# Kernel tuning notes

Hardware: AMD Instinct MI355X
Metric: run time of the kernel (lower is better)

## Reference

```python
import jax, jax.numpy as jnp
import numpy as np

N_SAMPLES = 128
AGENTS = 64
D = 128          # latent_size
EDIM = 2         # edge attr dim
N = N_SAMPLES * AGENTS
EPS = 1e-5


def _build_edges():
    a = np.arange(AGENTS)
    rows = np.repeat(a, AGENTS)
    cols = np.tile(a, AGENTS)
    mask = rows != cols  # fully connected, no self loops
    rows, cols = rows[mask], cols[mask]
    offsets = (np.arange(N_SAMPLES) * AGENTS)[:, None]
    src = (rows[None, :] + offsets).ravel().astype(np.int32)  # edge_index[0]
    dst = (cols[None, :] + offsets).ravel().astype(np.int32)  # edge_index[1]
    return src, dst


def setup_inputs() -> dict:
    key = jax.random.key(0)
    ks = jax.random.split(key, 16)
    src, dst = _build_edges()
    zin = 2 * D + EDIM  # CGConv concat [x_i, x_j, e]
    inp = {
        "gnn_in": jax.random.normal(ks[0], (N, D), jnp.float32),
        "centers": jax.random.normal(ks[1], (N, EDIM), jnp.float32),
        "edge_src": jnp.asarray(src),
        "edge_dst": jnp.asarray(dst),
    }
    for li, base in ((1, 2), (2, 8)):
        inp[f"Wf{li}"] = jax.random.normal(ks[base + 0], (zin, D), jnp.float32) / np.sqrt(zin)
        inp[f"bf{li}"] = jnp.zeros((D,), jnp.float32)
        inp[f"Ws{li}"] = jax.random.normal(ks[base + 1], (zin, D), jnp.float32) / np.sqrt(zin)
        inp[f"bs{li}"] = jnp.zeros((D,), jnp.float32)
        inp[f"gamma{li}"] = jnp.ones((D,), jnp.float32)
        inp[f"beta{li}"] = jnp.zeros((D,), jnp.float32)
    return inp


def _cgconv(x, e, src, dst, Wf, bf, Ws, bs, gamma, beta):
    # message: z = [x_i(target), x_j(source), e]; sigmoid(Wf z) * softplus(Ws z)
    z = jnp.concatenate([x[dst], x[src], e], axis=-1)  # [E, 2D+2]
    m = jax.nn.sigmoid(z @ Wf + bf) * jax.nn.softplus(z @ Ws + bs)
    agg = jax.ops.segment_sum(m, dst, num_segments=N)  # scatter-add at targets
    # batch norm (training-mode batch stats) then residual, as in PyG CGConv
    mu = agg.mean(axis=0)
    var = agg.var(axis=0)
    agg = (agg - mu) * jax.lax.rsqrt(var + EPS) * gamma + beta
    return agg + x


def reference(gnn_in, centers, edge_src, edge_dst,
              Wf1, bf1, Ws1, bs1, gamma1, beta1,
              Wf2, bf2, Ws2, bs2, gamma2, beta2):
    # edge_attr = centers[col] - centers[row]
    e = centers[edge_dst] - centers[edge_src]  # [E, 2]
    x = jax.nn.relu(_cgconv(gnn_in, e, edge_src, edge_dst, Wf1, bf1, Ws1, bs1, gamma1, beta1))
    x = jax.nn.relu(_cgconv(x, e, edge_src, edge_dst, Wf2, bf2, Ws2, bs2, gamma2, beta2))
    return x
```

## Files before the change

### kernel.cpp

```cpp
#include <hip/hip_runtime.h>
#include <hip/hip_bf16.h>

#define NSAMP 128
#define AGENTS 64
#define D 128
#define NN (NSAMP * AGENTS)
#define LOG2E 1.44269504088896340736f
#define LN2   0.69314718055994530942f
#define EPSF  1e-5f

typedef __attribute__((ext_vector_type(8))) short short8;
typedef __attribute__((ext_vector_type(4))) float floatx4;

__device__ __forceinline__ float u2f(unsigned v) {
    float f; __builtin_memcpy(&f, &v, 4); return f;
}
__device__ __forceinline__ unsigned f2u(float f) {
    unsigned v; __builtin_memcpy(&v, &f, 4); return v;
}
__device__ __forceinline__ unsigned short f2bf(float f) {
    unsigned x; __builtin_memcpy(&x, &f, 4);
    return (unsigned short)((x + 0x7FFFu + ((x >> 16) & 1u)) >> 16);
}

__global__ __launch_bounds__(256) void cvt_kernel(
    const float* __restrict__ Wf1, const float* __restrict__ Ws1,
    const float* __restrict__ Wf2, const float* __restrict__ Ws2,
    unsigned short* __restrict__ WT, float* __restrict__ sacc)
{
    int b = blockIdx.x;
    if (b < 64) {
        int rr = b * 16 + (threadIdx.x >> 4);
        int kk = (threadIdx.x & 15) * 8;
        int layer = rr >> 9, rem = rr & 511, arr = rem >> 7, c = rem & 127;
        const float* M = (arr < 2) ? (layer ? Wf2 : Wf1) : (layer ? Ws2 : Ws1);
        int side = arr & 1;
        short8 s;
        #pragma unroll
        for (int j = 0; j < 8; ++j)
            s[j] = (short)f2bf(M[(size_t)(side * 128 + kk + j) * D + c]);
        *(short8*)&WT[(size_t)(layer * 4 + arr) * 16384 + c * 128 + kk] = s;
    } else {
        sacc[threadIdx.x]       = 0.f;
        sacc[256 + threadIdx.x] = 0.f;
    }
}

__device__ __forceinline__ void stats_tree(
    unsigned int (*EApk)[17], unsigned int (*EBpk)[17],
    int cl, int slot, int c, float s1, float s2, float* __restrict__ sc)
{
    __syncthreads();
    EApk[slot][cl] = f2u(s1);
    EBpk[slot][cl] = f2u(s2);
    __syncthreads();
    #pragma unroll
    for (int off = 8; off >= 1; off >>= 1) {
        if (slot < off) {
            EApk[slot][cl] = f2u(u2f(EApk[slot][cl]) + u2f(EApk[slot + off][cl]));
            EBpk[slot][cl] = f2u(u2f(EBpk[slot][cl]) + u2f(EBpk[slot + off][cl]));
        }
        __syncthreads();
    }
    if (slot == 0) {
        atomicAdd(&sc[c],       u2f(EApk[0][cl]));
        atomicAdd(&sc[128 + c], u2f(EBpk[0][cl]));
    }
}

template<int LAYER>
__global__ __launch_bounds__(256, 4) void prep_half(
    const float* __restrict__ xin,
    const float* __restrict__ agg_in,
    const unsigned short* __restrict__ WT,
    const float* __restrict__ centers,
    const float* __restrict__ Wf, const float* __restrict__ bf_,
    const float* __restrict__ Ws, const float* __restrict__ bs_,
    const float* __restrict__ gm_prev, const float* __restrict__ bt_prev,
    const float* __restrict__ sacc_prev,
    float* __restrict__ agg_out, float* __restrict__ sacc_out)
{
    const int bid = blockIdx.x;
    const int xcd = bid & 7;
    const int tmp = bid >> 3;
    const int inner = tmp & 15;
    const int s = ((tmp >> 4) << 3) + xcd;
    const int q = inner >> 1, h = inner & 1;

    const int nbase = s * AGENTS;
    const int tid = threadIdx.x, w = tid >> 6, lane = tid & 63;
    const int quad = lane >> 4, l16 = lane & 15;
    const int col = q * 16 + l16;

    __shared__ unsigned int EApk[32][17];
    __shared__ unsigned int EBpk[64][17];
    __shared__ float bnA[128], bnB[128];

    if (LAYER == 2) {
        if (tid < 128) {
            const float inv = 1.f / NN;
            float mu = sacc_prev[tid] * inv;
            float var = sacc_prev[128 + tid] * inv - mu * mu;
            float rs = rsqrtf(var + EPSF);
            float A = rs * gm_prev[tid];
            bnA[tid] = A;
            bnB[tid] = fmaf(-mu, A, bt_prev[tid]);
        }
        __syncthreads();
    }

    short8 a[4];
    if (LAYER == 1) {
        const float* xr = xin + (size_t)(nbase + w * 16 + l16) * D + quad * 8;
        #pragma unroll
        for (int kc = 0; kc < 4; ++kc) {
            float4 v0 = *(const float4*)(xr + kc * 32);
            float4 v1 = *(const float4*)(xr + kc * 32 + 4);
            short8 t;
            t[0] = (short)f2bf(v0.x); t[1] = (short)f2bf(v0.y);
            t[2] = (short)f2bf(v0.z); t[3] = (short)f2bf(v0.w);
            t[4] = (short)f2bf(v1.x); t[5] = (short)f2bf(v1.y);
            t[6] = (short)f2bf(v1.z); t[7] = (short)f2bf(v1.w);
            a[kc] = t;
        }
    } else {
        const size_t ro = (size_t)(nbase + w * 16 + l16) * D + quad * 8;
        #pragma unroll
        for (int kc = 0; kc < 4; ++kc) {
            int cc = quad * 8 + kc * 32;
            float4 g0 = *(const float4*)&agg_in[ro + kc * 32];
            float4 g1 = *(const float4*)&agg_in[ro + kc * 32 + 4];
            float4 x0v = *(const float4*)(xin + ro + kc * 32);
            float4 x1v = *(const float4*)(xin + ro + kc * 32 + 4);
            float4 A0 = *(const float4*)&bnA[cc], A1 = *(const float4*)&bnA[cc + 4];
            float4 B0 = *(const float4*)&bnB[cc], B1 = *(const float4*)&bnB[cc + 4];
            short8 t;
            t[0] = (short)f2bf(fmaxf(0.f, fmaf(g0.x, A0.x, B0.x) + x0v.x));
            t[1] = (short)f2bf(fmaxf(0.f, fmaf(g0.y, A0.y, B0.y) + x0v.y));
            t[2] = (short)f2bf(fmaxf(0.f, fmaf(g0.z, A0.z, B0.z) + x0v.z));
            t[3] = (short)f2bf(fmaxf(0.f, fmaf(g0.w, A0.w, B0.w) + x0v.w));
            t[4] = (short)f2bf(fmaxf(0.f, fmaf(g1.x, A1.x, B1.x) + x1v.x));
            t[5] = (short)f2bf(fmaxf(0.f, fmaf(g1.y, A1.y, B1.y) + x1v.y));
            t[6] = (short)f2bf(fmaxf(0.f, fmaf(g1.z, A1.z, B1.z) + x1v.z));
            t[7] = (short)f2bf(fmaxf(0.f, fmaf(g1.w, A1.w, B1.w) + x1v.w));
            a[kc] = t;
        }
    }

    const int doEA = ((w >> 1) == h);
    floatx4 accB[2];
    #pragma unroll
    for (int a2 = 0; a2 < 2; ++a2) {
        const int arr = 1 + 2 * a2;
        const unsigned short* wp = WT + ((size_t)arr * 128 + col) * 128 + quad * 8;
        floatx4 ac = {0.f, 0.f, 0.f, 0.f};
        #pragma unroll
        for (int kc = 0; kc < 4; ++kc)
            ac = __builtin_amdgcn_mfma_f32_16x16x32_bf16(
                a[kc], *(const short8*)(wp + kc * 32), ac, 0, 0, 0);
        accB[a2] = ac;
    }
    floatx4 accA[2] = {{0,0,0,0},{0,0,0,0}};
    if (doEA) {
        #pragma unroll
        for (int a2 = 0; a2 < 2; ++a2) {
            const int arr = 2 * a2;
            const unsigned short* wp = WT + ((size_t)arr * 128 + col) * 128 + quad * 8;
            floatx4 ac = {0.f, 0.f, 0.f, 0.f};
            #pragma unroll
            for (int kc = 0; kc < 4; ++kc)
                ac = __builtin_amdgcn_mfma_f32_16x16x32_bf16(
                    a[kc], *(const short8*)(wp + kc * 32), ac, 0, 0, 0);
            accA[a2] = ac;
        }
    }
    const float cwf0 = Wf[256 * D + col], cwf1 = Wf[257 * D + col];
    const float cws0 = Ws[256 * D + col], cws1 = Ws[257 * D + col];
    const float bfv = bf_[col], bsv = bs_[col];
    #pragma unroll
    for (int r = 0; r < 4; ++r) {
        int row = w * 16 + quad * 4 + r;
        int n = nbase + row;
        float ce0 = centers[2 * n], ce1 = centers[2 * n + 1];
        float ctf = fmaf(ce0, cwf0, ce1 * cwf1);
        float cts = fmaf(ce0, cws0, ce1 * cws1);
        unsigned ebf = (unsigned)f2bf(__builtin_amdgcn_exp2f(-LOG2E * (accB[0][r] - ctf)));
        unsigned ebs = (unsigned)f2bf(__builtin_amdgcn_exp2f( LOG2E * (accB[1][r] - cts)));
        EBpk[row][l16] = ebf | (ebs << 16);
        if (doEA) {
            unsigned eaf = (unsigned)f2bf(__builtin_amdgcn_exp2f(-LOG2E * (accA[0][r] + ctf + bfv)));
            unsigned eas = (unsigned)f2bf(__builtin_amdgcn_exp2f( LOG2E * (accA[1][r] + cts + bsv)));
            EApk[(w & 1) * 16 + quad * 4 + r][l16] = eaf | (eas << 16);
        }
    }
    __syncthreads();

    const int cl = tid & 15, slot = tid >> 4;
    const int c = q * 16 + cl;
    float eaf[2], eas[2], ac2[2];
    #pragma unroll
    for (int i = 0; i < 2; ++i) {
        unsigned pk = EApk[slot * 2 + i][cl];
        eaf[i] = u2f(pk << 16);
        eas[i] = u2f(pk & 0xFFFF0000u);
        ac2[i] = 0.f;
    }
    #pragma unroll
    for (int jb = 0; jb < 64; jb += 8) {
        float ebf[8], ebs[8];
        #pragma unroll
        for (int u = 0; u < 8; ++u) {
            unsigned pk = EBpk[jb + u][cl];
            ebf[u] = u2f(pk << 16);
            ebs[u] = u2f(pk & 0xFFFF0000u);
        }
        float sg[16], lg[16];
        #pragma unroll
        for (int u = 0; u < 8; ++u) {
            sg[u * 2 + 0] = __builtin_amdgcn_rcpf(fmaf(eaf[0], ebf[u], 1.f));
            sg[u * 2 + 1] = __builtin_amdgcn_rcpf(fmaf(eaf[1], ebf[u], 1.f));
            lg[u * 2 + 0] = __builtin_amdgcn_logf(fmaf(eas[0], ebs[u], 1.f));
            lg[u * 2 + 1] = __builtin_amdgcn_logf(fmaf(eas[1], ebs[u], 1.f));
        }
        #pragma unroll
        for (int u = 0; u < 8; ++u) {
            ac2[0] = fmaf(sg[u * 2 + 0], lg[u * 2 + 0], ac2[0]);
            ac2[1] = fmaf(sg[u * 2 + 1], lg[u * 2 + 1], ac2[1]);
        }
    }
    float s1 = 0.f, s2 = 0.f;
    #pragma unroll
    for (int i = 0; i < 2; ++i) {
        int d = h * 32 + slot * 2 + i;
        unsigned pk = EBpk[d][cl];
        float ebf = u2f(pk << 16);
        float ebs = u2f(pk & 0xFFFF0000u);
        float sg = __builtin_amdgcn_rcpf(fmaf(eaf[i], ebf, 1.f));
        float lg = __builtin_amdgcn_logf(fmaf(eas[i], ebs, 1.f));
        float v = (ac2[i] - sg * lg) * LN2;
        agg_out[(size_t)(nbase + d) * D + c] = v;
        s1 += v; s2 += v * v;
    }
    stats_tree(EApk, EBpk, cl, slot, c, s1, s2, sacc_out);
}

__global__ __launch_bounds__(256) void final_bn(
    const float* __restrict__ x0, const float* __restrict__ agg1,
    const float* __restrict__ agg2, const float* __restrict__ sacc,
    const float* __restrict__ gm1, const float* __restrict__ bt1,
    const float* __restrict__ gm2, const float* __restrict__ bt2,
    float* __restrict__ outp)
{
    const int tid = threadIdx.x;
    __shared__ float bnA[128], bnB[128], bn2A[128], bn2B[128];
    if (tid < 128) {
        const float inv = 1.f / NN;
        float mu = sacc[tid] * inv;
        float var = sacc[128 + tid] * inv - mu * mu;
        float rs = rsqrtf(var + EPSF);
        float A = rs * gm1[tid];
        bnA[tid] = A;
        bnB[tid] = fmaf(-mu, A, bt1[tid]);
        float mu2 = sacc[256 + tid] * inv;
        float var2 = sacc[384 + tid] * inv - mu2 * mu2;
        float rs2 = rsqrtf(var2 + EPSF);
        float A2 = rs2 * gm2[tid];
        bn2A[tid] = A2;
        bn2B[tid] = fmaf(-mu2, A2, bt2[tid]);
    }
    __syncthreads();
    const int bid = blockIdx.x;
    const int s = ((bid >> 5) << 3) + (bid & 7);
    const int inner = (bid >> 3) & 3;
    const int t = (s * 4 + inner) * 256 + tid;
    const int n = t >> 4, c8 = (t & 15) * 8;
    size_t off = (size_t)n * D + c8;
    float o[8];
    #pragma unroll
    for (int hh = 0; hh < 2; ++hh) {
        float4 g2 = *(const float4*)&agg2[off + hh * 4];
        float4 g1 = *(const float4*)&agg1[off + hh * 4];
        float4 xv = *(const float4*)&x0[off + hh * 4];
        int cc = c8 + hh * 4;
        o[hh*4+0] = fmaxf(0.f, fmaf(g2.x, bn2A[cc+0], bn2B[cc+0]) +
                    fmaxf(0.f, fmaf(g1.x, bnA[cc+0], bnB[cc+0]) + xv.x));
        o[hh*4+1] = fmaxf(0.f, fmaf(g2.y, bn2A[cc+1], bn2B[cc+1]) +
                    fmaxf(0.f, fmaf(g1.y, bnA[cc+1], bnB[cc+1]) + xv.y));
        o[hh*4+2] = fmaxf(0.f, fmaf(g2.z, bn2A[cc+2], bn2B[cc+2]) +
                    fmaxf(0.f, fmaf(g1.z, bnA[cc+2], bnB[cc+2]) + xv.z));
        o[hh*4+3] = fmaxf(0.f, fmaf(g2.w, bn2A[cc+3], bn2B[cc+3]) +
                    fmaxf(0.f, fmaf(g1.w, bnA[cc+3], bnB[cc+3]) + xv.w));
    }
    *(float4*)&outp[off]     = *(float4*)&o[0];
    *(float4*)&outp[off + 4] = *(float4*)&o[4];
}

extern "C" void kernel_launch(void* const* d_in, const int* in_sizes, int n_in,
                              void* d_out, int out_size, void* d_ws, size_t ws_size,
                              hipStream_t stream) {
    const float* x0      = (const float*)d_in[0];
    const float* centers = (const float*)d_in[1];
    const float* Wf1 = (const float*)d_in[4];
    const float* bf1 = (const float*)d_in[5];
    const float* Ws1 = (const float*)d_in[6];
    const float* bs1 = (const float*)d_in[7];
    const float* gm1 = (const float*)d_in[8];
    const float* bt1 = (const float*)d_in[9];
    const float* Wf2 = (const float*)d_in[10];
    const float* bf2 = (const float*)d_in[11];
    const float* Ws2 = (const float*)d_in[12];
    const float* bs2 = (const float*)d_in[13];
    const float* gm2 = (const float*)d_in[14];
    const float* bt2 = (const float*)d_in[15];

    const size_t ND = (size_t)NN * D;
    unsigned short* WT = (unsigned short*)d_ws;
    float* fbase = (float*)(WT + 2 * 65536);
    float* agg1  = fbase;
    float* agg2  = fbase + ND;
    float* sacc  = fbase + 2 * ND;
    float* outp  = (float*)d_out;

    cvt_kernel<<<dim3(65), dim3(256), 0, stream>>>(
        Wf1, Ws1, Wf2, Ws2, WT, sacc);

    prep_half<1><<<dim3(2048), dim3(256), 0, stream>>>(
        x0, agg1 , WT, centers, Wf1, bf1, Ws1, bs1,
        gm1 , bt1 , sacc , agg1, sacc);

    prep_half<2><<<dim3(2048), dim3(256), 0, stream>>>(
        x0, agg1, WT + 65536, centers, Wf2, bf2, Ws2, bs2,
        gm1, bt1, sacc, agg2, sacc + 256);

    final_bn<<<dim3(512), dim3(256), 0, stream>>>(
        x0, agg1, agg2, sacc, gm1, bt1, gm2, bt2, outp);
}
```

Baseline: 162.6 us.

## Fuse weight bf16 conversion into conv kernels via LDS staging, drop cvt kernel

Removes the separate weight-transpose/convert kernel. Each prep_half block now loads its 16-column fp32 weight slice, converts it to bf16 and stages it in shared memory, and the MFMA B operands read from LDS instead of a global bf16 buffer. The stats accumulator is zeroed with hipMemsetAsync instead of inside that kernel. The sigmoid/softplus inner loop is restructured to precompute its arguments, with rcp/log issued through inline asm. The trade is one fewer launch in exchange for redundant strided fp32 weight loads in each of the 2048 blocks per layer, plus extra LDS use and a barrier.

New measurement: 150.5 us. -7.4%, faster.

```diff
diff --git a/kernel.cpp b/kernel.cpp
--- a/kernel.cpp
+++ b/kernel.cpp
@@ -23,29 +23,6 @@
     return (unsigned short)((x + 0x7FFFu + ((x >> 16) & 1u)) >> 16);
 }
 
-__global__ __launch_bounds__(256) void cvt_kernel(
-    const float* __restrict__ Wf1, const float* __restrict__ Ws1,
-    const float* __restrict__ Wf2, const float* __restrict__ Ws2,
-    unsigned short* __restrict__ WT, float* __restrict__ sacc)
-{
-    int b = blockIdx.x;
-    if (b < 64) {
-        int rr = b * 16 + (threadIdx.x >> 4);
-        int kk = (threadIdx.x & 15) * 8;
-        int layer = rr >> 9, rem = rr & 511, arr = rem >> 7, c = rem & 127;
-        const float* M = (arr < 2) ? (layer ? Wf2 : Wf1) : (layer ? Ws2 : Ws1);
-        int side = arr & 1;
-        short8 s;
-        #pragma unroll
-        for (int j = 0; j < 8; ++j)
-            s[j] = (short)f2bf(M[(size_t)(side * 128 + kk + j) * D + c]);
-        *(short8*)&WT[(size_t)(layer * 4 + arr) * 16384 + c * 128 + kk] = s;
-    } else {
-        sacc[threadIdx.x]       = 0.f;
-        sacc[256 + threadIdx.x] = 0.f;
-    }
-}
-
 __device__ __forceinline__ void stats_tree(
     unsigned int (*EApk)[17], unsigned int (*EBpk)[17],
     int cl, int slot, int c, float s1, float s2, float* __restrict__ sc)
@@ -72,7 +49,6 @@
 __global__ __launch_bounds__(256, 4) void prep_half(
     const float* __restrict__ xin,
     const float* __restrict__ agg_in,
-    const unsigned short* __restrict__ WT,
     const float* __restrict__ centers,
     const float* __restrict__ Wf, const float* __restrict__ bf_,
     const float* __restrict__ Ws, const float* __restrict__ bs_,
@@ -92,10 +68,25 @@
     const int quad = lane >> 4, l16 = lane & 15;
     const int col = q * 16 + l16;
 
+    __shared__ __align__(16) unsigned short WL[4][16][136];
     __shared__ unsigned int EApk[32][17];
     __shared__ unsigned int EBpk[64][17];
     __shared__ float bnA[128], bnB[128];
 
+    {
+        const int arr = tid >> 6, klane = tid & 63;
+        const int wcol = klane & 15, kg = klane >> 4;
+        const float* M = (arr < 2) ? Wf : Ws;
+        const int side = arr & 1;
+        const float* src = M + (size_t)(side * 128 + kg * 32) * D + q * 16 + wcol;
+        #pragma unroll
+        for (int u = 0; u < 16; ++u) {
+            float f0 = src[(size_t)(2 * u) * D];
+            float f1 = src[(size_t)(2 * u + 1) * D];
+            unsigned pk = (unsigned)f2bf(f0) | ((unsigned)f2bf(f1) << 16);
+            *(unsigned*)&WL[arr][wcol][kg * 32 + 2 * u] = pk;
+        }
+    }
     if (LAYER == 2) {
         if (tid < 128) {
             const float inv = 1.f / NN;
@@ -106,8 +97,8 @@
             bnA[tid] = A;
             bnB[tid] = fmaf(-mu, A, bt_prev[tid]);
         }
-        __syncthreads();
-    }
+    }
+    __syncthreads();
 
     short8 a[4];
     if (LAYER == 1) {
@@ -152,12 +143,11 @@
     #pragma unroll
     for (int a2 = 0; a2 < 2; ++a2) {
         const int arr = 1 + 2 * a2;
-        const unsigned short* wp = WT + ((size_t)arr * 128 + col) * 128 + quad * 8;
         floatx4 ac = {0.f, 0.f, 0.f, 0.f};
         #pragma unroll
         for (int kc = 0; kc < 4; ++kc)
             ac = __builtin_amdgcn_mfma_f32_16x16x32_bf16(
-                a[kc], *(const short8*)(wp + kc * 32), ac, 0, 0, 0);
+                a[kc], *(const short8*)&WL[arr][l16][quad * 8 + kc * 32], ac, 0, 0, 0);
         accB[a2] = ac;
     }
     floatx4 accA[2] = {{0,0,0,0},{0,0,0,0}};
@@ -165,12 +155,11 @@
         #pragma unroll
         for (int a2 = 0; a2 < 2; ++a2) {
             const int arr = 2 * a2;
-            const unsigned short* wp = WT + ((size_t)arr * 128 + col) * 128 + quad * 8;
             floatx4 ac = {0.f, 0.f, 0.f, 0.f};
             #pragma unroll
             for (int kc = 0; kc < 4; ++kc)
                 ac = __builtin_amdgcn_mfma_f32_16x16x32_bf16(
-                    a[kc], *(const short8*)(wp + kc * 32), ac, 0, 0, 0);
+                    a[kc], *(const short8*)&WL[arr][l16][quad * 8 + kc * 32], ac, 0, 0, 0);
             accA[a2] = ac;
         }
     }
@@ -207,26 +196,26 @@
     }
     #pragma unroll
     for (int jb = 0; jb < 64; jb += 8) {
-        float ebf[8], ebs[8];
+        float af[16], as_[16];
         #pragma unroll
         for (int u = 0; u < 8; ++u) {
             unsigned pk = EBpk[jb + u][cl];
-            ebf[u] = u2f(pk << 16);
-            ebs[u] = u2f(pk & 0xFFFF0000u);
+            float ebf = u2f(pk << 16);
+            float ebs = u2f(pk & 0xFFFF0000u);
+            af[u * 2 + 0] = fmaf(eaf[0], ebf, 1.f);
+            af[u * 2 + 1] = fmaf(eaf[1], ebf, 1.f);
+            as_[u * 2 + 0] = fmaf(eas[0], ebs, 1.f);
+            as_[u * 2 + 1] = fmaf(eas[1], ebs, 1.f);
         }
         float sg[16], lg[16];
         #pragma unroll
-        for (int u = 0; u < 8; ++u) {
-            sg[u * 2 + 0] = __builtin_amdgcn_rcpf(fmaf(eaf[0], ebf[u], 1.f));
-            sg[u * 2 + 1] = __builtin_amdgcn_rcpf(fmaf(eaf[1], ebf[u], 1.f));
-            lg[u * 2 + 0] = __builtin_amdgcn_logf(fmaf(eas[0], ebs[u], 1.f));
-            lg[u * 2 + 1] = __builtin_amdgcn_logf(fmaf(eas[1], ebs[u], 1.f));
-        }
-        #pragma unroll
-        for (int u = 0; u < 8; ++u) {
-            ac2[0] = fmaf(sg[u * 2 + 0], lg[u * 2 + 0], ac2[0]);
-            ac2[1] = fmaf(sg[u * 2 + 1], lg[u * 2 + 1], ac2[1]);
-        }
+        for (int u = 0; u < 16; ++u) {
+            asm volatile("v_rcp_f32 %0, %1" : "=v"(sg[u]) : "v"(af[u]));
+            asm volatile("v_log_f32 %0, %1" : "=v"(lg[u]) : "v"(as_[u]));
+        }
+        #pragma unroll
+        for (int u = 0; u < 16; ++u)
+            ac2[u & 1] = fmaf(sg[u], lg[u], ac2[u & 1]);
     }
     float s1 = 0.f, s2 = 0.f;
     #pragma unroll
@@ -314,22 +303,19 @@
     const float* bt2 = (const float*)d_in[15];
 
     const size_t ND = (size_t)NN * D;
-    unsigned short* WT = (unsigned short*)d_ws;
-    float* fbase = (float*)(WT + 2 * 65536);
-    float* agg1  = fbase;
-    float* agg2  = fbase + ND;
-    float* sacc  = fbase + 2 * ND;
-    float* outp  = (float*)d_out;
-
-    cvt_kernel<<<dim3(65), dim3(256), 0, stream>>>(
-        Wf1, Ws1, Wf2, Ws2, WT, sacc);
+    float* agg1 = (float*)d_ws;
+    float* agg2 = agg1 + ND;
+    float* sacc = agg1 + 2 * ND;
+    float* outp = (float*)d_out;
+
+    hipMemsetAsync(sacc, 0, 512 * sizeof(float), stream);
 
     prep_half<1><<<dim3(2048), dim3(256), 0, stream>>>(
-        x0, agg1 , WT, centers, Wf1, bf1, Ws1, bs1,
+        x0, agg1 , centers, Wf1, bf1, Ws1, bs1,
         gm1 , bt1 , sacc , agg1, sacc);
 
     prep_half<2><<<dim3(2048), dim3(256), 0, stream>>>(
-        x0, agg1, WT + 65536, centers, Wf2, bf2, Ws2, bs2,
+        x0, agg1, centers, Wf2, bf2, Ws2, bs2,
         gm1, bt1, sacc, agg2, sacc + 256);
 
     final_bn<<<dim3(512), dim3(256), 0, stream>>>(
```
